# Kernel optimization log

Hardware: AMD Instinct MI355X
Metric: run time of the kernel (lower is better)

The kernel has to match this reference:

```python
import jax, jax.numpy as jnp
import numpy as np

D_MODEL = 1024
N_HEADS = 16
D_K = 64
D_V = 64
B = 2
S = 2048


def setup_inputs() -> dict:
    key = jax.random.key(0)
    ks = jax.random.split(key, 7)
    q = jax.random.normal(ks[0], (B, S, D_MODEL), dtype=jnp.float32)
    k = jax.random.normal(ks[1], (B, S, D_MODEL), dtype=jnp.float32)
    v = jax.random.normal(ks[2], (B, S, D_MODEL), dtype=jnp.float32)
    mask = jnp.ones((B, S, S), dtype=bool)
    sc = 1.0 / np.sqrt(D_MODEL)
    Wq = jax.random.normal(ks[3], (D_MODEL, N_HEADS * D_K), dtype=jnp.float32) * sc
    Wk = jax.random.normal(ks[4], (D_MODEL, N_HEADS * D_K), dtype=jnp.float32) * sc
    Wv = jax.random.normal(ks[5], (D_MODEL, N_HEADS * D_V), dtype=jnp.float32) * sc
    Wo = jax.random.normal(ks[6], (N_HEADS * D_V, D_MODEL), dtype=jnp.float32) * sc
    return {"q": q, "k": k, "v": v, "mask": mask,
            "Wq": Wq, "Wk": Wk, "Wv": Wv, "Wo": Wo}


def reference(q, k, v, mask, Wq, Wk, Wv, Wo):
    # projections (no bias)
    qh = (q @ Wq).reshape(B, S, N_HEADS, D_K).transpose(0, 2, 1, 3)  # [B,H,Sq,dk]
    kh = (k @ Wk).reshape(B, S, N_HEADS, D_K).transpose(0, 2, 1, 3)  # [B,H,Sk,dk]
    vh = (v @ Wv).reshape(B, S, N_HEADS, D_V).transpose(0, 2, 1, 3)  # [B,H,Sk,dv]
    # NOTE: original module does NOT scale by 1/sqrt(d_k)
    scores = jnp.einsum('bhqd,bhkd->bhqk', qh, kh)  # [B,H,Sq,Sk]
    scores = jnp.where(mask[:, None, :, :], scores, -jnp.inf)
    attn = jax.nn.softmax(scores, axis=-1)
    # dropout p=0.0 -> identity (eval mode)
    out = jnp.einsum('bhqk,bhkd->bhqd', attn, vh)  # [B,H,Sq,dv]
    out = out.transpose(0, 2, 1, 3).reshape(B, S, N_HEADS * D_V)
    return out @ Wo  # [B,S,d_model]
```

## Files before the change

### kernel.cpp

```cpp
#include <hip/hip_runtime.h>

typedef _Float16 half_t;
typedef _Float16 half8 __attribute__((ext_vector_type(8)));
typedef _Float16 half4 __attribute__((ext_vector_type(4)));
typedef float f32x4 __attribute__((ext_vector_type(4)));
typedef short short4v __attribute__((ext_vector_type(4)));
typedef unsigned int uint2v __attribute__((ext_vector_type(2)));
typedef unsigned short ushort4v __attribute__((ext_vector_type(4)));
typedef unsigned short ushort8 __attribute__((ext_vector_type(8)));

#define LOG2E 1.4426950408889634f

#define MFMA16_BF16(A, B, C) __builtin_amdgcn_mfma_f32_16x16x16bf16_1k((A), (B), (C), 0, 0, 0)

__device__ __forceinline__ void gl2lds16(const void* g, void* l) {
    __builtin_amdgcn_global_load_lds(
        (const __attribute__((address_space(1))) void*)g,
        (__attribute__((address_space(3))) void*)l, 16, 0, 0);
}

__device__ __forceinline__ unsigned pk_bf16(float a, float b) {
    unsigned ua = __builtin_bit_cast(unsigned, a) + 0x8000u;
    unsigned ub = __builtin_bit_cast(unsigned, b) + 0x8000u;
    return (ua >> 16) | (ub & 0xFFFF0000u);
}

__device__ __forceinline__ unsigned short bf16_bits(float a) {
    return (unsigned short)((__builtin_bit_cast(unsigned, a) + 0x8000u) >> 16);
}

__global__ __launch_bounds__(256) void prep_kernel(
    const float* __restrict__ q, const float* __restrict__ k,
    const float* __restrict__ v,
    const float* __restrict__ W0, const float* __restrict__ W1,
    const float* __restrict__ W2, const float* __restrict__ W3,
    half_t* __restrict__ X, half_t* __restrict__ WqkvT, half_t* __restrict__ WoT)
{
    __shared__ __attribute__((aligned(16))) float T[64][65];
    const int bid = blockIdx.x;
    if (bid < 12288) {
        size_t t = (size_t)bid * 256 + threadIdx.x;
        size_t e = t * 4;
        int id = (int)(e >> 22);
        const float* src = (id == 0) ? q : (id == 1) ? k : v;
        size_t off = e & ((1u << 22) - 1);
        float4 f = *(const float4*)(src + off);
        half4 hv = { (half_t)f.x, (half_t)f.y, (half_t)f.z, (half_t)f.w };
        *(half4*)(X + e) = hv;
        return;
    }
    const int bid2 = bid - 12288;
    const int z = bid2 >> 8;
    const int y = (bid2 >> 4) & 15;
    const int x = bid2 & 15;
    const float* W = (z == 0) ? W0 : (z == 1) ? W1 : (z == 2) ? W2 : W3;
    half_t* D = (z == 0) ? WqkvT : (z == 1) ? WqkvT + 1048576
              : (z == 2) ? WqkvT + 2097152 : WoT;
    const float sc = (z == 0) ? LOG2E : 1.0f;
    const int r0 = y * 64;
    const int c0 = x * 64;
    const int tid = threadIdx.x;
    const int tr = tid >> 4;
    const int tc = (tid & 15) * 4;
#pragma unroll
    for (int p = 0; p < 4; ++p) {
        int r = p * 16 + tr;
        float4 f = *(const float4*)(W + (size_t)(r0 + r) * 1024 + c0 + tc);
        T[r][tc + 0] = f.x; T[r][tc + 1] = f.y; T[r][tc + 2] = f.z; T[r][tc + 3] = f.w;
    }
    __syncthreads();
#pragma unroll
    for (int p = 0; p < 4; ++p) {
        int n = p * 16 + tr;
        half4 hv = { (half_t)(T[tc + 0][n] * sc), (half_t)(T[tc + 1][n] * sc),
                     (half_t)(T[tc + 2][n] * sc), (half_t)(T[tc + 3][n] * sc) };
        *(half4*)(D + (size_t)(c0 + n) * 1024 + r0 + tc) = hv;
    }
}

__global__ __launch_bounds__(256) void gemm_qkv_kernel(
    const half_t* __restrict__ A,
    const half_t* __restrict__ Bt0, const half_t* __restrict__ Bt1,
    const half_t* __restrict__ Bt2,
    half_t* __restrict__ C, unsigned short* __restrict__ VhtOut)
{
    __shared__ __attribute__((aligned(16))) char smem[32768];
    const int tid = threadIdx.x;
    const int lane = tid & 63;
    const int w = tid >> 6;
    const int quad = lane >> 4;
    const int l16 = lane & 15;
    const int wm = w >> 1, wn = w & 1;
    const int N = 1024;

    const int m0 = blockIdx.x * 128;
    const int n0 = blockIdx.y * 128;
    const int slab = blockIdx.x >> 5;
    const half_t* Bt = (slab == 0) ? Bt0 : (slab == 1) ? Bt1 : Bt2;

    const half_t* gA0 = A + (size_t)(m0 + (tid >> 2)) * 1024 + (tid & 3) * 8;
    const half_t* gA1 = A + (size_t)(m0 + 64 + (tid >> 2)) * 1024 + (tid & 3) * 8;
    const half_t* gB0 = Bt + (size_t)(n0 + (tid >> 2)) * 1024 + (tid & 3) * 8;
    const half_t* gB1 = Bt + (size_t)(n0 + 64 + (tid >> 2)) * 1024 + (tid & 3) * 8;
    const int lA0 = tid * 16, lA1 = (tid + 256) * 16;
    const int lB0 = 8192 + tid * 16, lB1 = 8192 + (tid + 256) * 16;

    f32x4 acc[4][4] = {};

    gl2lds16(gA0, smem + lA0); gl2lds16(gA1, smem + lA1);
    gl2lds16(gB0, smem + lB0); gl2lds16(gB1, smem + lB1);
    gA0 += 32; gA1 += 32; gB0 += 32; gB1 += 32;

    for (int kt = 0; kt < 32; ++kt) {
        __syncthreads();
        const int cur = (kt & 1) * 16384;
        if (kt < 31) {
            const int nxt = 16384 - cur;
            gl2lds16(gA0, smem + nxt + lA0); gl2lds16(gA1, smem + nxt + lA1);
            gl2lds16(gB0, smem + nxt + lB0); gl2lds16(gB1, smem + nxt + lB1);
            gA0 += 32; gA1 += 32; gB0 += 32; gB1 += 32;
        }
        const half_t* As = (const half_t*)(smem + cur);
        const half_t* Bs = (const half_t*)(smem + cur + 8192);
        half8 af[4], bf[4];
#pragma unroll
        for (int mt = 0; mt < 4; ++mt)
            af[mt] = *(const half8*)&As[(wm * 64 + mt * 16 + l16) * 32 + quad * 8];
#pragma unroll
        for (int nt = 0; nt < 4; ++nt)
            bf[nt] = *(const half8*)&Bs[(wn * 64 + nt * 16 + l16) * 32 + quad * 8];
#pragma unroll
        for (int mt = 0; mt < 4; ++mt)
#pragma unroll
            for (int nt = 0; nt < 4; ++nt)
                acc[mt][nt] = __builtin_amdgcn_mfma_f32_16x16x32_f16(
                    af[mt], bf[nt], acc[mt][nt], 0, 0, 0);
    }

    if (slab < 2) {
#pragma unroll
        for (int mt = 0; mt < 4; ++mt) {
            int rbase = m0 + wm * 64 + mt * 16 + quad * 4;
#pragma unroll
            for (int nt = 0; nt < 4; ++nt) {
                int col = n0 + wn * 64 + nt * 16 + l16;
#pragma unroll
                for (int r = 0; r < 4; ++r)
                    C[(size_t)(rbase + r) * N + col] = (half_t)acc[mt][nt][r];
            }
        }
    } else {
        unsigned short* Tr = (unsigned short*)smem;
        const int tok0 = m0 - 8192;
        const int bb = tok0 >> 11;
        const int ss0 = tok0 & 2047;
#pragma unroll
        for (int p = 0; p < 2; ++p) {
            __syncthreads();
#pragma unroll
            for (int t16 = 0; t16 < 2; ++t16) {
                int nt = 2 * p + t16;
                int c = wn * 32 + t16 * 16 + l16;
#pragma unroll
                for (int mt = 0; mt < 4; ++mt) {
                    int sb = wm * 64 + mt * 16 + quad * 4;
                    ushort4v pk = { bf16_bits(acc[mt][nt][0]), bf16_bits(acc[mt][nt][1]),
                                    bf16_bits(acc[mt][nt][2]), bf16_bits(acc[mt][nt][3]) };
                    *(ushort4v*)&Tr[c * 136 + sb] = pk;
                }
            }
            __syncthreads();
            int cc = tid >> 2, seg = tid & 3;
            int colit = ((cc >> 5) << 6) + 32 * p + (cc & 31);
            int ncol = n0 + colit;
            int row_out = ((bb << 4) + (ncol >> 6)) * 64 + (ncol & 63);
            unsigned short* gdst = VhtOut + (size_t)row_out * 2048 + ss0 + seg * 32;
            const unsigned short* lsrc = Tr + cc * 136 + seg * 32;
#pragma unroll
            for (int u = 0; u < 4; ++u)
                *(ushort8*)(gdst + u * 8) = *(const ushort8*)(lsrc + u * 8);
        }
    }
}

__global__ __launch_bounds__(256) void gemm_bt_m64_kernel(
    const half_t* __restrict__ A, const half_t* __restrict__ Bt,
    float* __restrict__ C)
{
    __shared__ __attribute__((aligned(16))) char smem[24576];
    const int tid = threadIdx.x;
    const int lane = tid & 63;
    const int w = tid >> 6;
    const int quad = lane >> 4;
    const int l16 = lane & 15;
    const int wm = w >> 1, wn = w & 1;
    const int N = 1024;

    const int m0 = blockIdx.x * 64;
    const int n0 = blockIdx.y * 128;

    const half_t* gA0 = A + (size_t)(m0 + (tid >> 2)) * 1024 + (tid & 3) * 8;
    const half_t* gB0 = Bt + (size_t)(n0 + (tid >> 2)) * 1024 + (tid & 3) * 8;
    const half_t* gB1 = Bt + (size_t)(n0 + 64 + (tid >> 2)) * 1024 + (tid & 3) * 8;
    const int lA0 = tid * 16;
    const int lB0 = 4096 + tid * 16, lB1 = 4096 + (tid + 256) * 16;

    f32x4 acc[2][4] = {};

    gl2lds16(gA0, smem + lA0);
    gl2lds16(gB0, smem + lB0); gl2lds16(gB1, smem + lB1);
    gA0 += 32; gB0 += 32; gB1 += 32;

    for (int kt = 0; kt < 32; ++kt) {
        __syncthreads();
        const int cur = (kt & 1) * 12288;
        if (kt < 31) {
            const int nxt = 12288 - cur;
            gl2lds16(gA0, smem + nxt + lA0);
            gl2lds16(gB0, smem + nxt + lB0); gl2lds16(gB1, smem + nxt + lB1);
            gA0 += 32; gB0 += 32; gB1 += 32;
        }
        const half_t* As = (const half_t*)(smem + cur);
        const half_t* Bs = (const half_t*)(smem + cur + 4096);
        half8 af[2], bf[4];
#pragma unroll
        for (int mt = 0; mt < 2; ++mt)
            af[mt] = *(const half8*)&As[(wm * 32 + mt * 16 + l16) * 32 + quad * 8];
#pragma unroll
        for (int nt = 0; nt < 4; ++nt)
            bf[nt] = *(const half8*)&Bs[(wn * 64 + nt * 16 + l16) * 32 + quad * 8];
#pragma unroll
        for (int mt = 0; mt < 2; ++mt)
#pragma unroll
            for (int nt = 0; nt < 4; ++nt)
                acc[mt][nt] = __builtin_amdgcn_mfma_f32_16x16x32_f16(
                    af[mt], bf[nt], acc[mt][nt], 0, 0, 0);
    }
#pragma unroll
    for (int mt = 0; mt < 2; ++mt) {
        int rbase = m0 + wm * 32 + mt * 16 + quad * 4;
#pragma unroll
        for (int nt = 0; nt < 4; ++nt) {
            int col = n0 + wn * 64 + nt * 16 + l16;
#pragma unroll
            for (int r = 0; r < 4; ++r)
                C[(size_t)(rbase + r) * N + col] = acc[mt][nt][r];
        }
    }
}

__global__ __launch_bounds__(256) void attn_kernel(
    const half_t* __restrict__ Qh, const half_t* __restrict__ Kh,
    const unsigned short* __restrict__ Vht, half_t* __restrict__ Out)
{
    __shared__ __attribute__((aligned(16))) char smem[32768];

    const int tid = threadIdx.x;
    const int lane = tid & 63;
    const int w = tid >> 6;
    const int quad = lane >> 4;
    const int l16 = lane & 15;
    const int swz = l16 & 7;

    const int bid = blockIdx.x;
    const int bh = bid & 31;
    const int qt = bid >> 5;
    const int h = bh & 15;
    const int b = bh >> 4;
    const int qrow0 = b * 2048 + qt * 128;
    const int qbase = qrow0 + w * 32;

    half8 qf[2][2];
#pragma unroll
    for (int qg = 0; qg < 2; ++qg)
#pragma unroll
        for (int ks = 0; ks < 2; ++ks)
            qf[qg][ks] = *(const half8*)(Qh + (size_t)(qbase + qg * 16 + l16) * 1024
                                         + h * 64 + ks * 32 + quad * 8);

    const half_t* kp0; const half_t* kp1;
    const unsigned short* vp0; const unsigned short* vp1;
    int ldk0, ldk1, ldv0, ldv1;
    {
        int c = tid;
        int r = c >> 3, g = (c & 7) ^ (r & 7);
        kp0 = Kh + (size_t)(b * 2048 + r) * 1024 + h * 64 + g * 8;
        ldk0 = c * 16;
        c = 256 + tid;
        r = c >> 3; g = (c & 7) ^ (r & 7);
        kp1 = Kh + (size_t)(b * 2048 + r) * 1024 + h * 64 + g * 8;
        ldk1 = c * 16;
        c = tid;
        r = c >> 3; g = (c & 7) ^ (r & 7);
        vp0 = Vht + (size_t)(bh * 64 + r) * 2048 + g * 8;
        ldv0 = 8192 + c * 16;
        c = 256 + tid;
        r = c >> 3; g = (c & 7) ^ (r & 7);
        vp1 = Vht + (size_t)(bh * 64 + r) * 2048 + g * 8;
        ldv1 = 8192 + c * 16;
    }

    f32x4 accT[2][4] = {};
    f32x4 accL[2] = {};
    const short4v ones = { 0x3F80, 0x3F80, 0x3F80, 0x3F80 };

    gl2lds16(kp0, (char*)smem + ldk0);
    gl2lds16(kp1, (char*)smem + ldk1);
    gl2lds16(vp0, (char*)smem + ldv0);
    gl2lds16(vp1, (char*)smem + ldv1);
    kp0 += 64 * 1024; kp1 += 64 * 1024; vp0 += 64; vp1 += 64;

    for (int kt = 0; kt < 32; ++kt) {
        __syncthreads();
        const int cur = (kt & 1) * 16384;
        if (kt < 31) {
            const int nxt = 16384 - cur;
            gl2lds16(kp0, (char*)smem + nxt + ldk0);
            gl2lds16(kp1, (char*)smem + nxt + ldk1);
            gl2lds16(vp0, (char*)smem + nxt + ldv0);
            gl2lds16(vp1, (char*)smem + nxt + ldv1);
            kp0 += 64 * 1024; kp1 += 64 * 1024; vp0 += 64; vp1 += 64;
        }
        const half_t* Ksp = (const half_t*)(smem + cur);
        const unsigned short* Vsp = (const unsigned short*)(smem + cur + 8192);

        short4v pb[2][4];
#pragma unroll
        for (int t = 0; t < 4; ++t) {
            half8 k0 = *(const half8*)&Ksp[(t * 16 + l16) * 64 + ((quad ^ swz) * 8)];
            half8 k1 = *(const half8*)&Ksp[(t * 16 + l16) * 64 + (((4 + quad) ^ swz) * 8)];
#pragma unroll
            for (int qg = 0; qg < 2; ++qg) {
                f32x4 z = {};
                z = __builtin_amdgcn_mfma_f32_16x16x32_f16(k0, qf[qg][0], z, 0, 0, 0);
                z = __builtin_amdgcn_mfma_f32_16x16x32_f16(k1, qf[qg][1], z, 0, 0, 0);
                float e0 = __builtin_amdgcn_exp2f(z[0]);
                float e1 = __builtin_amdgcn_exp2f(z[1]);
                float e2 = __builtin_amdgcn_exp2f(z[2]);
                float e3 = __builtin_amdgcn_exp2f(z[3]);
                uint2v dd = { pk_bf16(e0, e1), pk_bf16(e2, e3) };
                pb[qg][t] = __builtin_bit_cast(short4v, dd);
            }
        }

#pragma unroll
        for (int t = 0; t < 4; ++t) {
#pragma unroll
            for (int dt = 0; dt < 4; ++dt) {
                int row = dt * 16 + l16;
                int ch = (t * 2 + (quad >> 1)) ^ swz;
                short4v vf = *(const short4v*)&Vsp[row * 64 + ch * 8 + (quad & 1) * 4];
                accT[0][dt] = MFMA16_BF16(vf, pb[0][t], accT[0][dt]);
                accT[1][dt] = MFMA16_BF16(vf, pb[1][t], accT[1][dt]);
            }
            accL[0] = MFMA16_BF16(ones, pb[0][t], accL[0]);
            accL[1] = MFMA16_BF16(ones, pb[1][t], accL[1]);
        }
    }

    __syncthreads();
    float inv0 = 1.0f / accL[0][0];
    float inv1 = 1.0f / accL[1][0];
    half_t* Ob = (half_t*)smem + w * (32 * 72);
#pragma unroll
    for (int qg = 0; qg < 2; ++qg) {
        float iv = qg ? inv1 : inv0;
#pragma unroll
        for (int dt = 0; dt < 4; ++dt) {
            f32x4 a = accT[qg][dt];
            half4 hv = { (half_t)(a[0] * iv), (half_t)(a[1] * iv),
                         (half_t)(a[2] * iv), (half_t)(a[3] * iv) };
            *(half4*)&Ob[(qg * 16 + l16) * 72 + dt * 16 + quad * 4] = hv;
        }
    }
    __syncthreads();
#pragma unroll
    for (int p = 0; p < 4; ++p) {
        int cid = p * 64 + lane;
        int row = cid >> 3, ch = cid & 7;
        half8 vv = *(const half8*)&Ob[row * 72 + ch * 8];
        *(half8*)(Out + (size_t)(qbase + row) * 1024 + h * 64 + ch * 8) = vv;
    }
}

extern "C" void kernel_launch(void* const* d_in, const int* in_sizes, int n_in,
                              void* d_out, int out_size, void* d_ws, size_t ws_size,
                              hipStream_t stream)
{
    const float* q  = (const float*)d_in[0];
    const float* k  = (const float*)d_in[1];
    const float* v  = (const float*)d_in[2];
    const float* Wq = (const float*)d_in[4];
    const float* Wk = (const float*)d_in[5];
    const float* Wv = (const float*)d_in[6];
    const float* Wo = (const float*)d_in[7];
    float* out = (float*)d_out;
    char* ws = (char*)d_ws;

    half_t* Xqkv    = (half_t*)(ws);
    half_t* AttnOut = (half_t*)(ws + 8388608);
    half_t* WqkvT   = (half_t*)(ws + 25165824);
    half_t* WoT     = (half_t*)(ws + 31457280);
    half_t* QKVh    = (half_t*)(ws + 33554432);
    unsigned short* Vht = (unsigned short*)(QKVh + (size_t)8192 * 1024);

    prep_kernel<<<13312, 256, 0, stream>>>(
        q, k, v, Wq, Wk, Wv, Wo, Xqkv, WqkvT, WoT);
    gemm_qkv_kernel<<<dim3(96, 8), 256, 0, stream>>>(
        Xqkv, WqkvT, WqkvT + 1024 * 1024, WqkvT + 2 * 1024 * 1024,
        QKVh, Vht);
    attn_kernel<<<512, 256, 0, stream>>>(
        QKVh, QKVh + (size_t)4096 * 1024, Vht, AttnOut);
    gemm_bt_m64_kernel<<<dim3(64, 8), 256, 0, stream>>>(
        AttnOut, WoT, out);
}
```

Baseline: 244.9 us.

## Swizzle GEMM LDS tiles, double attention KV tile to 128, use perm for bf16 pack

The two projection GEMMs now XOR-swizzle the 16-byte chunk index within each 32-element LDS row, on both the global-to-LDS copy and the fragment reads, to reduce LDS bank conflicts. The attention kernel doubles its K/V tile from 64 to 128 keys per iteration, so it runs half as many barrier-separated iterations; this doubles LDS to 64 KB per block, which can lower occupancy. The bf16 packing helper now uses a single v_perm instruction in place of a shift, mask and or.

```diff
diff --git a/kernel.cpp b/kernel.cpp
--- a/kernel.cpp
+++ b/kernel.cpp
@@ -22,7 +22,7 @@
 __device__ __forceinline__ unsigned pk_bf16(float a, float b) {
     unsigned ua = __builtin_bit_cast(unsigned, a) + 0x8000u;
     unsigned ub = __builtin_bit_cast(unsigned, b) + 0x8000u;
-    return (ua >> 16) | (ub & 0xFFFF0000u);
+    return __builtin_amdgcn_perm(ub, ua, 0x07060302u);
 }
 
 __device__ __forceinline__ unsigned short bf16_bits(float a) {
@@ -91,6 +91,7 @@
     const int quad = lane >> 4;
     const int l16 = lane & 15;
     const int wm = w >> 1, wn = w & 1;
+    const int swz4 = l16 & 3;
     const int N = 1024;
 
     const int m0 = blockIdx.x * 128;
@@ -98,10 +99,11 @@
     const int slab = blockIdx.x >> 5;
     const half_t* Bt = (slab == 0) ? Bt0 : (slab == 1) ? Bt1 : Bt2;
 
-    const half_t* gA0 = A + (size_t)(m0 + (tid >> 2)) * 1024 + (tid & 3) * 8;
-    const half_t* gA1 = A + (size_t)(m0 + 64 + (tid >> 2)) * 1024 + (tid & 3) * 8;
-    const half_t* gB0 = Bt + (size_t)(n0 + (tid >> 2)) * 1024 + (tid & 3) * 8;
-    const half_t* gB1 = Bt + (size_t)(n0 + 64 + (tid >> 2)) * 1024 + (tid & 3) * 8;
+    int cA0 = tid, cA1 = tid + 256;
+    const half_t* gA0 = A + (size_t)(m0 + (cA0 >> 2)) * 1024 + (((cA0 & 3) ^ ((cA0 >> 2) & 3)) * 8);
+    const half_t* gA1 = A + (size_t)(m0 + (cA1 >> 2)) * 1024 + (((cA1 & 3) ^ ((cA1 >> 2) & 3)) * 8);
+    const half_t* gB0 = Bt + (size_t)(n0 + (cA0 >> 2)) * 1024 + (((cA0 & 3) ^ ((cA0 >> 2) & 3)) * 8);
+    const half_t* gB1 = Bt + (size_t)(n0 + (cA1 >> 2)) * 1024 + (((cA1 & 3) ^ ((cA1 >> 2) & 3)) * 8);
     const int lA0 = tid * 16, lA1 = (tid + 256) * 16;
     const int lB0 = 8192 + tid * 16, lB1 = 8192 + (tid + 256) * 16;
 
@@ -125,10 +127,10 @@
         half8 af[4], bf[4];
 #pragma unroll
         for (int mt = 0; mt < 4; ++mt)
-            af[mt] = *(const half8*)&As[(wm * 64 + mt * 16 + l16) * 32 + quad * 8];
+            af[mt] = *(const half8*)&As[(wm * 64 + mt * 16 + l16) * 32 + ((quad ^ swz4) * 8)];
 #pragma unroll
         for (int nt = 0; nt < 4; ++nt)
-            bf[nt] = *(const half8*)&Bs[(wn * 64 + nt * 16 + l16) * 32 + quad * 8];
+            bf[nt] = *(const half8*)&Bs[(wn * 64 + nt * 16 + l16) * 32 + ((quad ^ swz4) * 8)];
 #pragma unroll
         for (int mt = 0; mt < 4; ++mt)
 #pragma unroll
@@ -194,14 +196,16 @@
     const int quad = lane >> 4;
     const int l16 = lane & 15;
     const int wm = w >> 1, wn = w & 1;
+    const int swz4 = l16 & 3;
     const int N = 1024;
 
     const int m0 = blockIdx.x * 64;
     const int n0 = blockIdx.y * 128;
 
-    const half_t* gA0 = A + (size_t)(m0 + (tid >> 2)) * 1024 + (tid & 3) * 8;
-    const half_t* gB0 = Bt + (size_t)(n0 + (tid >> 2)) * 1024 + (tid & 3) * 8;
-    const half_t* gB1 = Bt + (size_t)(n0 + 64 + (tid >> 2)) * 1024 + (tid & 3) * 8;
+    int c0 = tid, c1 = tid + 256;
+    const half_t* gA0 = A + (size_t)(m0 + (c0 >> 2)) * 1024 + (((c0 & 3) ^ ((c0 >> 2) & 3)) * 8);
+    const half_t* gB0 = Bt + (size_t)(n0 + (c0 >> 2)) * 1024 + (((c0 & 3) ^ ((c0 >> 2) & 3)) * 8);
+    const half_t* gB1 = Bt + (size_t)(n0 + (c1 >> 2)) * 1024 + (((c1 & 3) ^ ((c1 >> 2) & 3)) * 8);
     const int lA0 = tid * 16;
     const int lB0 = 4096 + tid * 16, lB1 = 4096 + (tid + 256) * 16;
 
@@ -225,10 +229,10 @@
         half8 af[2], bf[4];
 #pragma unroll
         for (int mt = 0; mt < 2; ++mt)
-            af[mt] = *(const half8*)&As[(wm * 32 + mt * 16 + l16) * 32 + quad * 8];
+            af[mt] = *(const half8*)&As[(wm * 32 + mt * 16 + l16) * 32 + ((quad ^ swz4) * 8)];
 #pragma unroll
         for (int nt = 0; nt < 4; ++nt)
-            bf[nt] = *(const half8*)&Bs[(wn * 64 + nt * 16 + l16) * 32 + quad * 8];
+            bf[nt] = *(const half8*)&Bs[(wn * 64 + nt * 16 + l16) * 32 + ((quad ^ swz4) * 8)];
 #pragma unroll
         for (int mt = 0; mt < 2; ++mt)
 #pragma unroll
@@ -253,7 +257,7 @@
     const half_t* __restrict__ Qh, const half_t* __restrict__ Kh,
     const unsigned short* __restrict__ Vht, half_t* __restrict__ Out)
 {
-    __shared__ __attribute__((aligned(16))) char smem[32768];
+    __shared__ __attribute__((aligned(16))) char smem[65536];
 
     const int tid = threadIdx.x;
     const int lane = tid & 63;
@@ -278,55 +282,48 @@
             qf[qg][ks] = *(const half8*)(Qh + (size_t)(qbase + qg * 16 + l16) * 1024
                                          + h * 64 + ks * 32 + quad * 8);
 
-    const half_t* kp0; const half_t* kp1;
-    const unsigned short* vp0; const unsigned short* vp1;
-    int ldk0, ldk1, ldv0, ldv1;
-    {
-        int c = tid;
-        int r = c >> 3, g = (c & 7) ^ (r & 7);
-        kp0 = Kh + (size_t)(b * 2048 + r) * 1024 + h * 64 + g * 8;
-        ldk0 = c * 16;
-        c = 256 + tid;
-        r = c >> 3; g = (c & 7) ^ (r & 7);
-        kp1 = Kh + (size_t)(b * 2048 + r) * 1024 + h * 64 + g * 8;
-        ldk1 = c * 16;
-        c = tid;
-        r = c >> 3; g = (c & 7) ^ (r & 7);
-        vp0 = Vht + (size_t)(bh * 64 + r) * 2048 + g * 8;
-        ldv0 = 8192 + c * 16;
-        c = 256 + tid;
-        r = c >> 3; g = (c & 7) ^ (r & 7);
-        vp1 = Vht + (size_t)(bh * 64 + r) * 2048 + g * 8;
-        ldv1 = 8192 + c * 16;
+    const half_t* kp[4]; const unsigned short* vp[4];
+    int ldk[4], ldv[4];
+#pragma unroll
+    for (int i = 0; i < 4; ++i) {
+        int c = i * 256 + tid;
+        int rK = c >> 3, gK = (c & 7) ^ (rK & 7);
+        kp[i] = Kh + (size_t)(b * 2048 + rK) * 1024 + h * 64 + gK * 8;
+        ldk[i] = c * 16;
+        int rV = c >> 4, gV = (c & 15) ^ (rV & 7);
+        vp[i] = Vht + (size_t)(bh * 64 + rV) * 2048 + gV * 8;
+        ldv[i] = 16384 + c * 16;
     }
 
     f32x4 accT[2][4] = {};
     f32x4 accL[2] = {};
     const short4v ones = { 0x3F80, 0x3F80, 0x3F80, 0x3F80 };
 
-    gl2lds16(kp0, (char*)smem + ldk0);
-    gl2lds16(kp1, (char*)smem + ldk1);
-    gl2lds16(vp0, (char*)smem + ldv0);
-    gl2lds16(vp1, (char*)smem + ldv1);
-    kp0 += 64 * 1024; kp1 += 64 * 1024; vp0 += 64; vp1 += 64;
-
-    for (int kt = 0; kt < 32; ++kt) {
+#pragma unroll
+    for (int i = 0; i < 4; ++i) {
+        gl2lds16(kp[i], (char*)smem + ldk[i]);
+        gl2lds16(vp[i], (char*)smem + ldv[i]);
+        kp[i] += 128 * 1024; vp[i] += 128;
+    }
+
+    for (int kt = 0; kt < 16; ++kt) {
         __syncthreads();
-        const int cur = (kt & 1) * 16384;
-        if (kt < 31) {
-            const int nxt = 16384 - cur;
-            gl2lds16(kp0, (char*)smem + nxt + ldk0);
-            gl2lds16(kp1, (char*)smem + nxt + ldk1);
-            gl2lds16(vp0, (char*)smem + nxt + ldv0);
-            gl2lds16(vp1, (char*)smem + nxt + ldv1);
-            kp0 += 64 * 1024; kp1 += 64 * 1024; vp0 += 64; vp1 += 64;
+        const int cur = (kt & 1) * 32768;
+        if (kt < 15) {
+            const int nxt = 32768 - cur;
+#pragma unroll
+            for (int i = 0; i < 4; ++i) {
+                gl2lds16(kp[i], (char*)smem + nxt + ldk[i]);
+                gl2lds16(vp[i], (char*)smem + nxt + ldv[i]);
+                kp[i] += 128 * 1024; vp[i] += 128;
+            }
         }
         const half_t* Ksp = (const half_t*)(smem + cur);
-        const unsigned short* Vsp = (const unsigned short*)(smem + cur + 8192);
-
-        short4v pb[2][4];
-#pragma unroll
-        for (int t = 0; t < 4; ++t) {
+        const unsigned short* Vsp = (const unsigned short*)(smem + cur + 16384);
+
+        short4v pb[2][8];
+#pragma unroll
+        for (int t = 0; t < 8; ++t) {
             half8 k0 = *(const half8*)&Ksp[(t * 16 + l16) * 64 + ((quad ^ swz) * 8)];
             half8 k1 = *(const half8*)&Ksp[(t * 16 + l16) * 64 + (((4 + quad) ^ swz) * 8)];
 #pragma unroll
@@ -344,12 +341,12 @@
         }
 
 #pragma unroll
-        for (int t = 0; t < 4; ++t) {
+        for (int t = 0; t < 8; ++t) {
 #pragma unroll
             for (int dt = 0; dt < 4; ++dt) {
                 int row = dt * 16 + l16;
                 int ch = (t * 2 + (quad >> 1)) ^ swz;
-                short4v vf = *(const short4v*)&Vsp[row * 64 + ch * 8 + (quad & 1) * 4];
+                short4v vf = *(const short4v*)&Vsp[row * 128 + ch * 8 + (quad & 1) * 4];
                 accT[0][dt] = MFMA16_BF16(vf, pb[0][t], accT[0][dt]);
                 accT[1][dt] = MFMA16_BF16(vf, pb[1][t], accT[1][dt]);
             }
```

After: 235.7 us. -3.8%, faster.
